# Kernel optimization log

Hardware: AMD Instinct MI355X
Metric: run time of the kernel (lower is better)

Reference implementation:

```python
import jax, jax.numpy as jnp
import numpy as np

HIDDEN = 1024
D_INNER = 2048      # expand * hidden
STATE = 16          # state_dim n
DT_RANK = 64        # ceil(hidden/16)
D_CONV = 4
B, S = 2, 2048
EPS = 1e-5


def setup_inputs() -> dict:
    key = jax.random.key(0)
    ks = jax.random.split(key, 10)
    sc = lambda fan_in: 1.0 / np.sqrt(fan_in)
    x = jax.random.normal(ks[0], (B, S, HIDDEN), dtype=jnp.float32)
    norm_w = jnp.ones((HIDDEN,), dtype=jnp.float32)
    in_proj_w = jax.random.uniform(ks[1], (2 * D_INNER, HIDDEN), minval=-sc(HIDDEN), maxval=sc(HIDDEN), dtype=jnp.float32)
    conv_w = jax.random.uniform(ks[2], (D_INNER, 1, D_CONV), minval=-sc(D_CONV), maxval=sc(D_CONV), dtype=jnp.float32)
    conv_b = jax.random.uniform(ks[3], (D_INNER,), minval=-sc(D_CONV), maxval=sc(D_CONV), dtype=jnp.float32)
    x_proj_w = jax.random.uniform(ks[4], (DT_RANK + 2 * STATE, D_INNER), minval=-sc(D_INNER), maxval=sc(D_INNER), dtype=jnp.float32)
    dt_proj_w = jax.random.uniform(ks[5], (D_INNER, DT_RANK), minval=-sc(DT_RANK), maxval=sc(DT_RANK), dtype=jnp.float32)
    dt_proj_b = jax.random.uniform(ks[6], (D_INNER,), minval=-sc(DT_RANK), maxval=sc(DT_RANK), dtype=jnp.float32)
    A_log = jnp.log(jnp.broadcast_to(jnp.arange(1, STATE + 1, dtype=jnp.float32), (D_INNER, STATE)))
    D = jnp.ones((D_INNER,), dtype=jnp.float32)
    out_proj_w = jax.random.uniform(ks[7], (HIDDEN, D_INNER), minval=-sc(D_INNER), maxval=sc(D_INNER), dtype=jnp.float32)
    return {"x": x, "norm_w": norm_w, "in_proj_w": in_proj_w, "conv_w": conv_w,
            "conv_b": conv_b, "x_proj_w": x_proj_w, "dt_proj_w": dt_proj_w,
            "dt_proj_b": dt_proj_b, "A_log": A_log, "D": D, "out_proj_w": out_proj_w}


def _selective_scan(u, delta, A, Bm, Cm, D):
    # u, delta: [b,s,d]; A: [d,n]; Bm, Cm: [b,s,n]; D: [d]
    deltaA = jnp.exp(jnp.einsum('bsd,dn->bsdn', delta, A))          # [b,s,d,n]
    deltaB_u = jnp.einsum('bsd,bsn,bsd->bsdn', delta, Bm, u)        # [b,s,d,n]

    def step(h, inp):
        dA_t, dBu_t, C_t = inp                                       # [b,d,n],[b,d,n],[b,n]
        h = dA_t * h + dBu_t
        y = jnp.einsum('bdn,bn->bd', h, C_t)
        return h, y

    h0 = jnp.zeros((u.shape[0], u.shape[2], A.shape[1]), dtype=u.dtype)
    _, ys = jax.lax.scan(step, h0,
                         (deltaA.transpose(1, 0, 2, 3),
                          deltaB_u.transpose(1, 0, 2, 3),
                          Cm.transpose(1, 0, 2)))
    y = ys.transpose(1, 0, 2)                                        # [b,s,d]
    return y + u * D


def reference(x, norm_w, in_proj_w, conv_w, conv_b, x_proj_w, dt_proj_w,
              dt_proj_b, A_log, D, out_proj_w):
    # RMSNorm
    xn = x * jax.lax.rsqrt(jnp.mean(x * x, axis=-1, keepdims=True) + EPS) * norm_w

    # in_proj -> split
    x_and_res = xn @ in_proj_w.T                                     # [b,s,2*d_inner]
    xi, res = jnp.split(x_and_res, 2, axis=-1)

    # causal depthwise conv1d (left-pad d_conv-1, truncate to s)
    xc = jax.lax.conv_general_dilated(
        xi.transpose(0, 2, 1), conv_w,
        window_strides=(1,), padding=[(D_CONV - 1, 0)],
        dimension_numbers=('NCH', 'OIH', 'NCH'),
        feature_group_count=D_INNER) + conv_b[None, :, None]
    xc = jax.nn.silu(xc.transpose(0, 2, 1))                          # [b,s,d_inner]

    # ssm
    A = -jnp.exp(A_log)
    x_dbl = xc @ x_proj_w.T                                          # [b,s,dt_rank+2n]
    dt, Bm, Cm = jnp.split(x_dbl, [DT_RANK, DT_RANK + STATE], axis=-1)
    delta = jax.nn.softplus(dt @ dt_proj_w.T + dt_proj_b)            # [b,s,d_inner]
    y = _selective_scan(xc, delta, A, Bm, Cm, D)

    y = y * jax.nn.silu(res)
    out = y @ out_proj_w.T
    return out + x
```

## Files before the change

### kernel.cpp

```cpp
#include <hip/hip_runtime.h>
#include <math.h>

#define HIDDEN   1024
#define D_INNER  2048
#define NSTATE   16
#define DT_RANK  64
#define BATCH    2
#define SEQ      2048
#define T_TOK    (BATCH * SEQ)
#define XDBL     (DT_RANK + 2 * NSTATE)
#define NCH      64
#define CHL      (SEQ / NCH)
#define BDN      (BATCH * D_INNER * NSTATE)

typedef float f32x4   __attribute__((ext_vector_type(4)));
typedef short bf16x8  __attribute__((ext_vector_type(8)));
typedef short short4v __attribute__((ext_vector_type(4)));

#define AS1 __attribute__((address_space(1)))
#define AS3 __attribute__((address_space(3)))
#define GLOAD(src, dst) __builtin_amdgcn_global_load_lds( \
    (const AS1 unsigned int*)(src), (AS3 unsigned int*)(dst), 16, 0, 0)

__device__ __forceinline__ float silu_f(float x) { return x / (1.0f + __expf(-x)); }
__device__ __forceinline__ float softplus_f(float x) {
    return fmaxf(x, 0.0f) + log1pf(__expf(-fabsf(x)));
}
__device__ __forceinline__ unsigned short f2bf(float x) {
    unsigned int u = __float_as_uint(x);
    u += 0x7fffu + ((u >> 16) & 1u);
    return (unsigned short)(u >> 16);
}
__device__ __forceinline__ float bf2f(unsigned short h) {
    return __uint_as_float(((unsigned int)h) << 16);
}

template<int SEGS>
__global__ __launch_bounds__(256) void wpack_kernel(
        const float* __restrict__ w, unsigned short* __restrict__ wp, int K) {
    int i = blockIdx.x * 256 + threadIdx.x;
    int kq = K >> 2;
    int row = i / kq;
    int c = (i - row * kq) << 2;
    float4 v = *(const float4*)(w + (size_t)row * K + c);
    short4v hi, lo;
    hi.x = f2bf(v.x); hi.y = f2bf(v.y); hi.z = f2bf(v.z); hi.w = f2bf(v.w);
    lo.x = f2bf(v.x - bf2f(hi.x)); lo.y = f2bf(v.y - bf2f(hi.y));
    lo.z = f2bf(v.z - bf2f(hi.z)); lo.w = f2bf(v.w - bf2f(hi.w));
    size_t b0 = (size_t)row * (SEGS * K) + c;
    *(short4v*)(wp + b0) = hi;
    if (SEGS == 2) *(short4v*)(wp + b0 + K) = lo;
}

__global__ __launch_bounds__(256) void rmsnorm_pack_kernel(
        const float* __restrict__ x, const float* __restrict__ w,
        unsigned short* __restrict__ xn_p) {
    int row = blockIdx.x;
    float4 v = ((const float4*)(x + (size_t)row * HIDDEN))[threadIdx.x];
    float ss = v.x*v.x + v.y*v.y + v.z*v.z + v.w*v.w;
    #pragma unroll
    for (int off = 32; off; off >>= 1) ss += __shfl_down(ss, off);
    __shared__ float wsum[4];
    if ((threadIdx.x & 63) == 0) wsum[threadIdx.x >> 6] = ss;
    __syncthreads();
    float scale = rsqrtf((wsum[0] + wsum[1] + wsum[2] + wsum[3]) / (float)HIDDEN + 1e-5f);
    float4 wv = ((const float4*)w)[threadIdx.x];
    float o0 = v.x * scale * wv.x, o1 = v.y * scale * wv.y;
    float o2 = v.z * scale * wv.z, o3 = v.w * scale * wv.w;
    short4v hi, lo;
    hi.x = f2bf(o0); hi.y = f2bf(o1); hi.z = f2bf(o2); hi.w = f2bf(o3);
    lo.x = f2bf(o0 - bf2f(hi.x)); lo.y = f2bf(o1 - bf2f(hi.y));
    lo.z = f2bf(o2 - bf2f(hi.z)); lo.w = f2bf(o3 - bf2f(hi.w));
    size_t b0 = (size_t)row * (2 * HIDDEN) + threadIdx.x * 4;
    *(short4v*)&xn_p[b0]          = hi;
    *(short4v*)&xn_p[b0 + HIDDEN] = lo;
}

template<int TERMS, int EPI>
__global__ __launch_bounds__(256) void mgemm_kernel(
        const unsigned short* __restrict__ Ap, const unsigned short* __restrict__ Wp,
        int Klog, int klen, int brows, float* __restrict__ C0, float* __restrict__ C1,
        int splitN, int ldout, size_t partStride, const float* __restrict__ bias) {
    constexpr int NT = (TERMS == 3) ? 4 : 3;
    __shared__ short lds[NT * 128 * 64];
    short* Ah = lds;
    short* Al = lds + 128 * 64;
    short* Bh = lds + 2 * 128 * 64;
    short* Bl = lds + 3 * 128 * 64;
    const int t = threadIdx.x;
    const int w = t >> 6, l = t & 63;
    const int m0 = blockIdx.y * 128, n0 = blockIdx.x * 128;
    const int kbeg = blockIdx.z * klen;
    const int wr = (w >> 1) * 64, wc = (w & 1) * 64;
    const int lrow = l & 15;
    f32x4 acc[4][4];
    #pragma unroll
    for (int m = 0; m < 4; ++m)
        #pragma unroll
        for (int n = 0; n < 4; ++n) {
            acc[m][n].x = 0.f; acc[m][n].y = 0.f; acc[m][n].z = 0.f; acc[m][n].w = 0.f;
        }
    const int Asr = 2 * Klog;
    const int Wsr = (TERMS == 3) ? 2 * Klog : Klog;
    const int srow = w * 32 + (l >> 3);
    const int sc8  = (l & 7) ^ ((l >> 3) & 7);
    const int brow = min(n0 + srow, brows - 1);
    const unsigned short* ga = Ap + (size_t)(m0 + srow) * Asr + sc8 * 8;
    const unsigned short* gb = Wp + (size_t)brow * Wsr + sc8 * 8;
    for (int k0 = kbeg; k0 < kbeg + klen; k0 += 64) {
        __syncthreads();
        #pragma unroll
        for (int q = 0; q < 4; ++q) {
            const int doff = (w * 32 + q * 8) * 128;
            GLOAD(ga + k0 + (size_t)q * 8 * Asr,        (char*)Ah + doff);
            GLOAD(ga + Klog + k0 + (size_t)q * 8 * Asr, (char*)Al + doff);
            GLOAD(gb + k0 + (size_t)q * 8 * Wsr,        (char*)Bh + doff);
            if (TERMS == 3)
                GLOAD(gb + Klog + k0 + (size_t)q * 8 * Wsr, (char*)Bl + doff);
        }
        __syncthreads();
        #pragma unroll
        for (int kk = 0; kk < 2; ++kk) {
            const int slot = ((kk * 4 + (l >> 4)) ^ (l & 7)) * 8;
            bf16x8 ah[4], al[4], bh[4], bl[4];
            #pragma unroll
            for (int m = 0; m < 4; ++m) {
                ah[m] = *(const bf16x8*)&Ah[(wr + m * 16 + lrow) * 64 + slot];
                al[m] = *(const bf16x8*)&Al[(wr + m * 16 + lrow) * 64 + slot];
            }
            #pragma unroll
            for (int n = 0; n < 4; ++n) {
                bh[n] = *(const bf16x8*)&Bh[(wc + n * 16 + lrow) * 64 + slot];
                if (TERMS == 3)
                    bl[n] = *(const bf16x8*)&Bl[(wc + n * 16 + lrow) * 64 + slot];
            }
            #pragma unroll
            for (int m = 0; m < 4; ++m)
                #pragma unroll
                for (int n = 0; n < 4; ++n) {
                    acc[m][n] = __builtin_amdgcn_mfma_f32_16x16x32_bf16(
                        ah[m], bh[n], acc[m][n], 0, 0, 0);
                    acc[m][n] = __builtin_amdgcn_mfma_f32_16x16x32_bf16(
                        al[m], bh[n], acc[m][n], 0, 0, 0);
                    if (TERMS == 3)
                        acc[m][n] = __builtin_amdgcn_mfma_f32_16x16x32_bf16(
                            ah[m], bl[n], acc[m][n], 0, 0, 0);
                }
        }
    }
    float* dst = (EPI == 2) ? (C0 + blockIdx.z * partStride) : C0;
    #pragma unroll
    for (int m = 0; m < 4; ++m) {
        #pragma unroll
        for (int n = 0; n < 4; ++n) {
            #pragma unroll
            for (int j = 0; j < 4; ++j) {
                int row = m0 + wr + m * 16 + (l >> 4) * 4 + j;
                int col = n0 + wc + n * 16 + (l & 15);
                float v = acc[m][n][j];
                if (EPI == 0) {
                    if (col < splitN) C0[(size_t)row * ldout + col] = v;
                    else              C1[(size_t)row * ldout + (col - splitN)] = v;
                } else if (EPI == 2) {
                    dst[(size_t)row * ldout + col] = v;
                } else {
                    C0[(size_t)row * ldout + col] = softplus_f(v + bias[col]);
                }
            }
        }
    }
}

__global__ __launch_bounds__(256) void reduce4_kernel(
        const float* __restrict__ parts, size_t partStride,
        const float* __restrict__ x, float* __restrict__ out) {
    size_t i = (size_t)blockIdx.x * 256 + threadIdx.x;
    float4 a = ((const float4*)(parts))[i];
    float4 b = ((const float4*)(parts + partStride))[i];
    float4 c = ((const float4*)(parts + 2 * partStride))[i];
    float4 d = ((const float4*)(parts + 3 * partStride))[i];
    float4 xv = ((const float4*)x)[i];
    float4 o;
    o.x = a.x + b.x + c.x + d.x + xv.x;
    o.y = a.y + b.y + c.y + d.y + xv.y;
    o.z = a.z + b.z + c.z + d.z + xv.z;
    o.w = a.w + b.w + c.w + d.w + xv.w;
    ((float4*)out)[i] = o;
}

__global__ __launch_bounds__(256) void reduceX_kernel(
        const float* __restrict__ parts, float* __restrict__ xdbl,
        unsigned short* __restrict__ dtp) {
    int i = blockIdx.x * 256 + threadIdx.x;
    int row = i / 24;
    int c = (i - row * 24) * 4;
    float4 a = *(const float4*)(parts + (size_t)row * 128 + c);
    float4 b = *(const float4*)(parts + 524288 + (size_t)row * 128 + c);
    float4 d = *(const float4*)(parts + 2 * 524288 + (size_t)row * 128 + c);
    float4 e = *(const float4*)(parts + 3 * 524288 + (size_t)row * 128 + c);
    float4 s;
    s.x = a.x + b.x + d.x + e.x;
    s.y = a.y + b.y + d.y + e.y;
    s.z = a.z + b.z + d.z + e.z;
    s.w = a.w + b.w + d.w + e.w;
    *(float4*)(xdbl + (size_t)row * XDBL + c) = s;
    if (c < DT_RANK) {
        short4v hi, lo;
        hi.x = f2bf(s.x); hi.y = f2bf(s.y); hi.z = f2bf(s.z); hi.w = f2bf(s.w);
        lo.x = f2bf(s.x - bf2f(hi.x)); lo.y = f2bf(s.y - bf2f(hi.y));
        lo.z = f2bf(s.z - bf2f(hi.z)); lo.w = f2bf(s.w - bf2f(hi.w));
        size_t b0 = (size_t)row * 128 + c;
        *(short4v*)(dtp + b0)      = hi;
        *(short4v*)(dtp + b0 + 64) = lo;
    }
}

__global__ __launch_bounds__(256) void conv_silu_kernel(
        const float* __restrict__ xi, const float* __restrict__ w,
        const float* __restrict__ b, unsigned short* __restrict__ xc_p) {
    size_t i = (size_t)blockIdx.x * 256 + threadIdx.x;
    int d = (int)(i & (D_INNER - 1));
    int tt = (int)(i >> 11);
    int s = tt & (SEQ - 1);
    float4 wv = ((const float4*)w)[d];
    float acc = b[d];
    if (s >= 3) acc += wv.x * xi[i - 3 * D_INNER];
    if (s >= 2) acc += wv.y * xi[i - 2 * D_INNER];
    if (s >= 1) acc += wv.z * xi[i - 1 * D_INNER];
    acc += wv.w * xi[i];
    float o = silu_f(acc);
    unsigned short hi = f2bf(o);
    unsigned short lo = f2bf(o - bf2f(hi));
    size_t o2 = (size_t)tt * (2 * D_INNER) + d;
    xc_p[o2]           = hi;
    xc_p[o2 + D_INNER] = lo;
}


__global__ __launch_bounds__(256) void scanA_kernel(
        const unsigned short* __restrict__ xcp, const float* __restrict__ delta,
        const float* __restrict__ xdbl, const float* __restrict__ A_log,
        float* __restrict__ hpart, float* __restrict__ Pp) {
    const int bid = blockIdx.x;
    const int b    = bid >> 9;
    const int c    = (bid >> 3) & 63;
    const int dblk = bid & 7;
    const int d    = (dblk << 8) + threadIdx.x;
    float adn[NSTATE];
    #pragma unroll
    for (int k = 0; k < 4; ++k) {
        float4 a = *(const float4*)(A_log + d * NSTATE + k * 4);
        adn[k*4+0] = -__expf(a.x); adn[k*4+1] = -__expf(a.y);
        adn[k*4+2] = -__expf(a.z); adn[k*4+3] = -__expf(a.w);
    }
    float h[NSTATE], P[NSTATE];
    #pragma unroll
    for (int n = 0; n < NSTATE; ++n) { h[n] = 0.f; P[n] = 1.f; }
    const int rowbase = b * SEQ + c * CHL;
    #pragma unroll 4
    for (int r = 0; r < CHL; ++r) {
        const int row = rowbase + r;
        const float* brow = xdbl + (size_t)row * XDBL + DT_RANK;
        size_t o2 = (size_t)row * (2 * D_INNER) + d;
        float dl = delta[(size_t)row * D_INNER + d];
        float u  = bf2f(xcp[o2]) + bf2f(xcp[o2 + D_INNER]);
        float du = dl * u;
        #pragma unroll
        for (int n = 0; n < NSTATE; ++n) {
            float dA = __expf(dl * adn[n]);
            h[n] = fmaf(dA, h[n], du * brow[n]);
            P[n] *= dA;
        }
    }
    size_t base = (size_t)c * BDN + (size_t)(b * D_INNER + d) * NSTATE;
    #pragma unroll
    for (int k = 0; k < 4; ++k) {
        *(float4*)(hpart + base + k * 4) = make_float4(h[k*4], h[k*4+1], h[k*4+2], h[k*4+3]);
        *(float4*)(Pp    + base + k * 4) = make_float4(P[k*4], P[k*4+1], P[k*4+2], P[k*4+3]);
    }
}

__global__ __launch_bounds__(256) void scanB_kernel(
        const float* __restrict__ hpart, const float* __restrict__ Pp,
        float* __restrict__ hstart) {
    int idx = blockIdx.x * 256 + threadIdx.x;
    float h = 0.f;
    for (int c = 0; c < NCH; ++c) {
        hstart[(size_t)c * BDN + idx] = h;
        h = fmaf(Pp[(size_t)c * BDN + idx], h, hpart[(size_t)c * BDN + idx]);
    }
}

__global__ __launch_bounds__(256) void scanC_kernel(
        const unsigned short* xcp, const float* __restrict__ delta,
        const float* __restrict__ xdbl, const float* __restrict__ A_log,
        const float* __restrict__ Dp, const float* __restrict__ hstart,
        const float* __restrict__ res, unsigned short* y_p) {
    const int bid = blockIdx.x;
    const int b    = bid >> 9;
    const int c    = (bid >> 3) & 63;
    const int dblk = bid & 7;
    const int d    = (dblk << 8) + threadIdx.x;
    float adn[NSTATE];
    #pragma unroll
    for (int k = 0; k < 4; ++k) {
        float4 a = *(const float4*)(A_log + d * NSTATE + k * 4);
        adn[k*4+0] = -__expf(a.x); adn[k*4+1] = -__expf(a.y);
        adn[k*4+2] = -__expf(a.z); adn[k*4+3] = -__expf(a.w);
    }
    const float Dd = Dp[d];
    float h[NSTATE];
    size_t base = (size_t)c * BDN + (size_t)(b * D_INNER + d) * NSTATE;
    #pragma unroll
    for (int k = 0; k < 4; ++k) {
        float4 hv = *(const float4*)(hstart + base + k * 4);
        h[k*4] = hv.x; h[k*4+1] = hv.y; h[k*4+2] = hv.z; h[k*4+3] = hv.w;
    }
    const int rowbase = b * SEQ + c * CHL;
    #pragma unroll 4
    for (int r = 0; r < CHL; ++r) {
        const int row = rowbase + r;
        const float* brow = xdbl + (size_t)row * XDBL + DT_RANK;
        const float* crow = brow + NSTATE;
        size_t o2 = (size_t)row * (2 * D_INNER) + d;
        float dl = delta[(size_t)row * D_INNER + d];
        float u  = bf2f(xcp[o2]) + bf2f(xcp[o2 + D_INNER]);
        float du = dl * u;
        float ys[4];
        ys[0] = u * Dd; ys[1] = 0.f; ys[2] = 0.f; ys[3] = 0.f;
        #pragma unroll
        for (int n = 0; n < NSTATE; ++n) {
            float dA = __expf(dl * adn[n]);
            h[n] = fmaf(dA, h[n], du * brow[n]);
            ys[n & 3] = fmaf(h[n], crow[n], ys[n & 3]);
        }
        float ysum = (ys[0] + ys[1]) + (ys[2] + ys[3]);
        float rv = res[(size_t)row * D_INNER + d];
        float gv = ysum * silu_f(rv);
        unsigned short hi = f2bf(gv);
        unsigned short lo = f2bf(gv - bf2f(hi));
        y_p[o2]           = hi;
        y_p[o2 + D_INNER] = lo;
    }
}

extern "C" void kernel_launch(void* const* d_in, const int* in_sizes, int n_in,
                              void* d_out, int out_size, void* d_ws, size_t ws_size,
                              hipStream_t stream) {
    const float* x         = (const float*)d_in[0];
    const float* norm_w    = (const float*)d_in[1];
    const float* in_proj_w = (const float*)d_in[2];
    const float* conv_w    = (const float*)d_in[3];
    const float* conv_b    = (const float*)d_in[4];
    const float* x_proj_w  = (const float*)d_in[5];
    const float* dt_proj_w = (const float*)d_in[6];
    const float* dt_proj_b = (const float*)d_in[7];
    const float* A_log     = (const float*)d_in[8];
    const float* Dp        = (const float*)d_in[9];
    const float* out_proj_w= (const float*)d_in[10];
    float* out = (float*)d_out;
    float* ws  = (float*)d_ws;

    const size_t M8 = (size_t)T_TOK * D_INNER;
    float* res   = ws;
    float* delta = res + M8;
    float* xdbl  = delta + M8;
    unsigned short* xn_p   = (unsigned short*)(xdbl + (size_t)T_TOK * XDBL);
    unsigned short* w_in_p = xn_p   + (size_t)4096 * 2048;
    unsigned short* w_out_p= w_in_p + (size_t)4096 * 1024;
    unsigned short* w_xp_p = w_out_p+ (size_t)1024 * 4096;
    unsigned short* w_dt_p = w_xp_p + (size_t)96 * 4096;
    unsigned short* xc_p   = w_dt_p + (size_t)2048 * 128;
    unsigned short* dtp_p  = xc_p   + (size_t)4096 * 4096;
    float* xi    = (float*)(dtp_p + (size_t)4096 * 128);
    float* hpart = xi;
    float* Pp    = xi + (size_t)BDN * NCH;
    float* hstart= (float*)xn_p;
    float* parts_x = delta;
    unsigned short* y_p = xc_p;
    float* parts = ws;
    const size_t partStride = (size_t)T_TOK * HIDDEN;

    wpack_kernel<1><<<4096, 256, 0, stream>>>(in_proj_w,  w_in_p,  HIDDEN);
    wpack_kernel<2><<<2048, 256, 0, stream>>>(out_proj_w, w_out_p, D_INNER);
    wpack_kernel<2><<<192,  256, 0, stream>>>(x_proj_w,   w_xp_p,  D_INNER);
    wpack_kernel<2><<<128,  256, 0, stream>>>(dt_proj_w,  w_dt_p,  DT_RANK);

    rmsnorm_pack_kernel<<<T_TOK, 256, 0, stream>>>(x, norm_w, xn_p);

    {
        dim3 g(4096 / 128, T_TOK / 128, 1);
        mgemm_kernel<2, 0><<<g, 256, 0, stream>>>(xn_p, w_in_p, HIDDEN, HIDDEN,
                                                  4096, xi, res, D_INNER, D_INNER, 0, nullptr);
    }

    conv_silu_kernel<<<(int)(M8 / 256), 256, 0, stream>>>(xi, conv_w, conv_b, xc_p);

    {
        dim3 g(1, T_TOK / 128, 4);
        mgemm_kernel<3, 2><<<g, 256, 0, stream>>>(xc_p, w_xp_p, D_INNER, D_INNER / 4,
                                                  96, parts_x, nullptr, 0, 128, 524288, nullptr);
    }
    reduceX_kernel<<<T_TOK * 24 / 256, 256, 0, stream>>>(parts_x, xdbl, dtp_p);

    {
        dim3 g(D_INNER / 128, T_TOK / 128, 1);
        mgemm_kernel<3, 3><<<g, 256, 0, stream>>>(dtp_p, w_dt_p, DT_RANK, DT_RANK,
                                                  D_INNER, delta, nullptr, 0, D_INNER, 0, dt_proj_b);
    }

    scanA_kernel<<<BATCH * NCH * 8, 256, 0, stream>>>(xc_p, delta, xdbl, A_log, hpart, Pp);
    scanB_kernel<<<BDN / 256, 256, 0, stream>>>(hpart, Pp, hstart);
    scanC_kernel<<<BATCH * NCH * 8, 256, 0, stream>>>(xc_p, delta, xdbl, A_log, Dp, hstart, res, y_p);

    {
        dim3 g(HIDDEN / 128, T_TOK / 128, 4);
        mgemm_kernel<3, 2><<<g, 256, 0, stream>>>(y_p, w_out_p, D_INNER, D_INNER / 4,
                                                  HIDDEN, parts, nullptr, 0, HIDDEN, partStride, nullptr);
    }
    reduce4_kernel<<<(int)(partStride / 4 / 256), 256, 0, stream>>>(parts, partStride, x, out);
}
```

Baseline: 336.2 us.

## Add dedicated 128x256 in_proj GEMM kernel and retune split-K factors

Replaces the generic in_proj GEMM with a specialized kernel that uses 128x256 tiles, direct global-to-LDS loads with swizzled slots, and launch bounds allowing two blocks per CU. This is meant to raise reuse of the A tiles and cut the epilogue branching. It also raises the x_proj split-K from 4 to 8 for more parallelism, and lowers the out_proj split-K from 4 to 2 so the partial-sum reduction moves less memory. Each 16x16 output tile holds 32 accumulator fragments, so register pressure is high and may limit occupancy.

```diff
diff --git a/kernel.cpp b/kernel.cpp
--- a/kernel.cpp
+++ b/kernel.cpp
@@ -74,6 +74,77 @@
     size_t b0 = (size_t)row * (2 * HIDDEN) + threadIdx.x * 4;
     *(short4v*)&xn_p[b0]          = hi;
     *(short4v*)&xn_p[b0 + HIDDEN] = lo;
+}
+
+__global__ __launch_bounds__(256, 2) void mgemm_in_kernel(
+        const unsigned short* __restrict__ Ap,
+        const unsigned short* __restrict__ Wp,
+        float* __restrict__ C0, float* __restrict__ C1) {
+    __shared__ short Ah[128 * 64];
+    __shared__ short Al[128 * 64];
+    __shared__ short Bh[256 * 64];
+    const int t = threadIdx.x;
+    const int w = t >> 6, l = t & 63;
+    const int m0 = blockIdx.y * 128, n0 = blockIdx.x * 256;
+    const int lrow = l & 15;
+    f32x4 acc[8][4];
+    #pragma unroll
+    for (int m = 0; m < 8; ++m)
+        #pragma unroll
+        for (int n = 0; n < 4; ++n) {
+            acc[m][n].x = 0.f; acc[m][n].y = 0.f; acc[m][n].z = 0.f; acc[m][n].w = 0.f;
+        }
+    const int srow8 = l >> 3;
+    const int sc8   = (l & 7) ^ srow8;
+    const unsigned short* ga = Ap + (size_t)(m0 + w * 32 + srow8) * 2048 + sc8 * 8;
+    const unsigned short* gb = Wp + (size_t)(n0 + w * 64 + srow8) * 1024 + sc8 * 8;
+    for (int k0 = 0; k0 < 1024; k0 += 64) {
+        __syncthreads();
+        #pragma unroll
+        for (int q = 0; q < 4; ++q) {
+            const int ar = (w * 32 + q * 8) * 128;
+            GLOAD(ga + k0 + (size_t)q * 8 * 2048,        (char*)Ah + ar);
+            GLOAD(ga + 1024 + k0 + (size_t)q * 8 * 2048, (char*)Al + ar);
+        }
+        #pragma unroll
+        for (int q = 0; q < 8; ++q)
+            GLOAD(gb + k0 + (size_t)q * 8 * 1024, (char*)Bh + (w * 64 + q * 8) * 128);
+        __syncthreads();
+        #pragma unroll
+        for (int kk = 0; kk < 2; ++kk) {
+            const int slot = ((kk * 4 + (l >> 4)) ^ (l & 7)) * 8;
+            bf16x8 bh[4];
+            #pragma unroll
+            for (int n = 0; n < 4; ++n)
+                bh[n] = *(const bf16x8*)&Bh[(w * 64 + n * 16 + lrow) * 64 + slot];
+            #pragma unroll
+            for (int m = 0; m < 8; ++m) {
+                bf16x8 ah = *(const bf16x8*)&Ah[(m * 16 + lrow) * 64 + slot];
+                bf16x8 al = *(const bf16x8*)&Al[(m * 16 + lrow) * 64 + slot];
+                #pragma unroll
+                for (int n = 0; n < 4; ++n) {
+                    acc[m][n] = __builtin_amdgcn_mfma_f32_16x16x32_bf16(
+                        ah, bh[n], acc[m][n], 0, 0, 0);
+                    acc[m][n] = __builtin_amdgcn_mfma_f32_16x16x32_bf16(
+                        al, bh[n], acc[m][n], 0, 0, 0);
+                }
+            }
+        }
+    }
+    float* dst = (n0 < D_INNER) ? C0 : C1;
+    const int cbase = (n0 < D_INNER) ? n0 : n0 - D_INNER;
+    #pragma unroll
+    for (int m = 0; m < 8; ++m) {
+        #pragma unroll
+        for (int n = 0; n < 4; ++n) {
+            #pragma unroll
+            for (int j = 0; j < 4; ++j) {
+                int row = m0 + m * 16 + (l >> 4) * 4 + j;
+                int col = cbase + w * 64 + n * 16 + (l & 15);
+                dst[(size_t)row * D_INNER + col] = acc[m][n][j];
+            }
+        }
+    }
 }
 
 template<int TERMS, int EPI>
@@ -158,10 +229,7 @@
                 int row = m0 + wr + m * 16 + (l >> 4) * 4 + j;
                 int col = n0 + wc + n * 16 + (l & 15);
                 float v = acc[m][n][j];
-                if (EPI == 0) {
-                    if (col < splitN) C0[(size_t)row * ldout + col] = v;
-                    else              C1[(size_t)row * ldout + (col - splitN)] = v;
-                } else if (EPI == 2) {
+                if (EPI == 2) {
                     dst[(size_t)row * ldout + col] = v;
                 } else {
                     C0[(size_t)row * ldout + col] = softplus_f(v + bias[col]);
@@ -171,20 +239,18 @@
     }
 }
 
-__global__ __launch_bounds__(256) void reduce4_kernel(
+__global__ __launch_bounds__(256) void reduce2_kernel(
         const float* __restrict__ parts, size_t partStride,
         const float* __restrict__ x, float* __restrict__ out) {
     size_t i = (size_t)blockIdx.x * 256 + threadIdx.x;
     float4 a = ((const float4*)(parts))[i];
     float4 b = ((const float4*)(parts + partStride))[i];
-    float4 c = ((const float4*)(parts + 2 * partStride))[i];
-    float4 d = ((const float4*)(parts + 3 * partStride))[i];
     float4 xv = ((const float4*)x)[i];
     float4 o;
-    o.x = a.x + b.x + c.x + d.x + xv.x;
-    o.y = a.y + b.y + c.y + d.y + xv.y;
-    o.z = a.z + b.z + c.z + d.z + xv.z;
-    o.w = a.w + b.w + c.w + d.w + xv.w;
+    o.x = a.x + b.x + xv.x;
+    o.y = a.y + b.y + xv.y;
+    o.z = a.z + b.z + xv.z;
+    o.w = a.w + b.w + xv.w;
     ((float4*)out)[i] = o;
 }
 
@@ -194,15 +260,12 @@
     int i = blockIdx.x * 256 + threadIdx.x;
     int row = i / 24;
     int c = (i - row * 24) * 4;
-    float4 a = *(const float4*)(parts + (size_t)row * 128 + c);
-    float4 b = *(const float4*)(parts + 524288 + (size_t)row * 128 + c);
-    float4 d = *(const float4*)(parts + 2 * 524288 + (size_t)row * 128 + c);
-    float4 e = *(const float4*)(parts + 3 * 524288 + (size_t)row * 128 + c);
-    float4 s;
-    s.x = a.x + b.x + d.x + e.x;
-    s.y = a.y + b.y + d.y + e.y;
-    s.z = a.z + b.z + d.z + e.z;
-    s.w = a.w + b.w + d.w + e.w;
+    float4 s = make_float4(0.f, 0.f, 0.f, 0.f);
+    #pragma unroll
+    for (int z = 0; z < 8; ++z) {
+        float4 a = *(const float4*)(parts + (size_t)z * 524288 + (size_t)row * 128 + c);
+        s.x += a.x; s.y += a.y; s.z += a.z; s.w += a.w;
+    }
     *(float4*)(xdbl + (size_t)row * XDBL + c) = s;
     if (c < DT_RANK) {
         short4v hi, lo;
@@ -389,16 +452,15 @@
     rmsnorm_pack_kernel<<<T_TOK, 256, 0, stream>>>(x, norm_w, xn_p);
 
     {
-        dim3 g(4096 / 128, T_TOK / 128, 1);
-        mgemm_kernel<2, 0><<<g, 256, 0, stream>>>(xn_p, w_in_p, HIDDEN, HIDDEN,
-                                                  4096, xi, res, D_INNER, D_INNER, 0, nullptr);
+        dim3 g(4096 / 256, T_TOK / 128, 1);
+        mgemm_in_kernel<<<g, 256, 0, stream>>>(xn_p, w_in_p, xi, res);
     }
 
     conv_silu_kernel<<<(int)(M8 / 256), 256, 0, stream>>>(xi, conv_w, conv_b, xc_p);
 
     {
-        dim3 g(1, T_TOK / 128, 4);
-        mgemm_kernel<3, 2><<<g, 256, 0, stream>>>(xc_p, w_xp_p, D_INNER, D_INNER / 4,
+        dim3 g(1, T_TOK / 128, 8);
+        mgemm_kernel<3, 2><<<g, 256, 0, stream>>>(xc_p, w_xp_p, D_INNER, D_INNER / 8,
                                                   96, parts_x, nullptr, 0, 128, 524288, nullptr);
     }
     reduceX_kernel<<<T_TOK * 24 / 256, 256, 0, stream>>>(parts_x, xdbl, dtp_p);
@@ -414,9 +476,9 @@
     scanC_kernel<<<BATCH * NCH * 8, 256, 0, stream>>>(xc_p, delta, xdbl, A_log, Dp, hstart, res, y_p);
 
     {
-        dim3 g(HIDDEN / 128, T_TOK / 128, 4);
-        mgemm_kernel<3, 2><<<g, 256, 0, stream>>>(y_p, w_out_p, D_INNER, D_INNER / 4,
+        dim3 g(HIDDEN / 128, T_TOK / 128, 2);
+        mgemm_kernel<3, 2><<<g, 256, 0, stream>>>(y_p, w_out_p, D_INNER, D_INNER / 2,
                                                   HIDDEN, parts, nullptr, 0, HIDDEN, partStride, nullptr);
     }
-    reduce4_kernel<<<(int)(partStride / 4 / 256), 256, 0, stream>>>(parts, partStride, x, out);
-}
+    reduce2_kernel<<<(int)(partStride / 4 / 256), 256, 0, stream>>>(parts, partStride, x, out);
+}
```

New measurement: 312.7 us. 1.07x faster.
